# Kernel tuning notes

Measured on AMD Instinct MI355X. Metric: run time of the kernel, lower is better.

## Reference

```python
import jax, jax.numpy as jnp
import numpy as np

D = 256        # embedding_dim
K = 4096       # num_embeddings
DECAY = 0.99
EPS = 1e-05
COMMIT = 0.25


def setup_inputs() -> dict:
    key = jax.random.key(0)
    kx, ke = jax.random.split(key)
    x = jax.random.normal(kx, (32, 1024, D), dtype=jnp.float32)
    # variance_scaling(scale=1.0, mode='fan_in', distribution='uniform') on (D, K): fan_in = D
    limit = np.sqrt(3.0 / D).astype(np.float32)
    embeddings = jax.random.uniform(ke, (D, K), dtype=jnp.float32, minval=-limit, maxval=limit)
    return {
        'x': x,
        'embeddings': embeddings,
        'ema_counter': jnp.zeros((), jnp.float32),
        'ema_hidden_cluster': jnp.zeros((K,), jnp.float32),
        'ema_hidden_dw': jnp.zeros((D, K), jnp.float32),
    }


def reference(x, embeddings, ema_counter, ema_hidden_cluster, ema_hidden_dw):
    flat = x.reshape(-1, D)  # [N, D]
    # squared euclidean distance to each code: [N, K]
    distance = (jnp.sum(flat ** 2, axis=1, keepdims=True)
                - 2.0 * jnp.matmul(flat, embeddings)
                + jnp.sum(embeddings ** 2, axis=0, keepdims=True))
    encoding_indices = jnp.argmax(-distance, axis=1)           # [N]
    encodings = jax.nn.one_hot(encoding_indices, K, dtype=distance.dtype)  # [N, K]
    idx = encoding_indices.reshape(x.shape[:-1])               # [B, T]
    quantized = jnp.take(embeddings.T, idx, axis=0)            # [B, T, D]

    e_latent_loss = jnp.mean((quantized - x) ** 2)
    q_latent_loss = jnp.mean((quantized - x) ** 2)
    vq_loss = q_latent_loss + COMMIT * e_latent_loss

    # EMA codebook update (training=True path); debiased EMA per the module
    counter = ema_counter + 1.0
    bias = 1.0 - jnp.power(DECAY, counter)
    cluster_hidden = ema_hidden_cluster * DECAY + jnp.sum(encodings, axis=0) * (1.0 - DECAY)
    cluster_avg = cluster_hidden / bias                         # [K]
    dw = jnp.matmul(flat.T, encodings)                          # [D, K]
    dw_hidden = ema_hidden_dw * DECAY + dw * (1.0 - DECAY)
    dw_avg = dw_hidden / bias                                   # [D, K]
    n = jnp.sum(cluster_avg)
    cluster_norm = (cluster_avg + EPS) / (n + K * EPS) * n
    new_embeddings = dw_avg / cluster_norm[None, :]             # [D, K]

    avg_probs = jnp.mean(encodings, axis=0)
    perplexity = jnp.exp(-jnp.sum(avg_probs * jnp.log(avg_probs + 1e-10)))
    return quantized, vq_loss, perplexity, idx, new_embeddings
```

## Files before the change

### kernel.cpp

```cpp
#include <hip/hip_runtime.h>
#include <math.h>

#define N_TOK 32768
#define DIM   256
#define KCODE 4096

#define WS_E2      0
#define WS_COUNTS  4096
#define WS_LOSSP   8192
#define WS_SCAL    8448
#define WS_CNORM   8512
#define WS_IDX     12608
#define WS_EHS     307520
#define WS_DWT     1356096
#define WS_CARRYV  2404672
#define WS_CARRYI  2437440
#define WS_OFFS    2470208
#define WS_WOFF    2474304

#define OUT_Q      0
#define OUT_LOSS   8388608
#define OUT_PERP   8388609
#define OUT_IDX    8388610
#define OUT_EMB    8421378

#define EH_PLANE   1048576
#define XH_PLANE   8388608

typedef _Float16 f16x8 __attribute__((ext_vector_type(8)));
typedef _Float16 f16x4 __attribute__((ext_vector_type(4)));
typedef float    f32x4 __attribute__((ext_vector_type(4)));

__global__ void k_e2(const float* __restrict__ emb, float* __restrict__ e2)
{
    int k  = blockIdx.x * 256 + threadIdx.x;
    int d0 = blockIdx.y * 32;
    float s = 0.0f;
#pragma unroll 8
    for (int d = 0; d < 32; ++d) {
        float v = emb[(size_t)(d0 + d) * KCODE + k];
        s += v * v;
    }
    atomicAdd(&e2[k], s);
}

__global__ void k_split_x(const float* __restrict__ x, unsigned short* __restrict__ xh)
{
    int i = (blockIdx.x * 256 + threadIdx.x) * 8;
    float4 f0 = *(const float4*)(x + i);
    float4 f1 = *(const float4*)(x + i + 4);
    float fv[8] = {f0.x, f0.y, f0.z, f0.w, f1.x, f1.y, f1.z, f1.w};
    f16x8 h1, h2;
#pragma unroll
    for (int j = 0; j < 8; ++j) {
        _Float16 a = (_Float16)fv[j];
        h1[j] = a;
        h2[j] = (_Float16)(fv[j] - (float)a);
    }
    *(f16x8*)((_Float16*)xh + i)            = h1;
    *(f16x8*)((_Float16*)xh + XH_PLANE + i) = h2;
}

__global__ void k_split_e(const float* __restrict__ emb, unsigned short* __restrict__ ehs_)
{
    __shared__ float tile[32][33];
    _Float16* ehs = (_Float16*)ehs_;
    int t  = threadIdx.x;
    int tx = t & 31, iy = t >> 5;
    int k0 = blockIdx.x * 32, d0 = blockIdx.y * 32;
#pragma unroll
    for (int j = 0; j < 4; ++j)
        tile[iy + 8 * j][tx] = emb[(size_t)(d0 + iy + 8 * j) * KCODE + k0 + tx];
    __syncthreads();
    int code = k0 + tx;
    size_t base = (size_t)(((code >> 8) * 8) + (d0 >> 5)) * 8192 + (code & 255) * 32 + iy * 4;
    f16x4 h1, h2;
#pragma unroll
    for (int j = 0; j < 4; ++j) {
        float v = tile[iy * 4 + j][tx];
        _Float16 a = (_Float16)v;
        h1[j] = a;
        h2[j] = (_Float16)(v - (float)a);
    }
    *(f16x4*)(ehs + base)            = h1;
    *(f16x4*)(ehs + EH_PLANE + base) = h2;
}

__global__ __launch_bounds__(256, 2)
void k_argmin(const unsigned short* __restrict__ xh_, const unsigned short* __restrict__ ehs_,
              const float* __restrict__ e2, int* __restrict__ idx_out,
              float* __restrict__ carryV, int* __restrict__ carryI,
              float* __restrict__ out_idxf, float* __restrict__ counts,
              int ct0, int phase)
{
    __shared__ __align__(16) _Float16 Ah[2][64][256];

    const _Float16* xh  = (const _Float16*)xh_;
    const _Float16* ehs = (const _Float16*)ehs_;

    const int t    = threadIdx.x;
    const int lane = t & 63, w = t >> 6;
    const int lo   = lane & 15, q = lane >> 4;
    const int row0 = blockIdx.x * 64;

    {
        int m = t >> 3, kb = (t & 7) * 32;
#pragma unroll
        for (int p = 0; p < 2; ++p)
#pragma unroll
            for (int rr = 0; rr < 2; ++rr) {
                int mm = m + 32 * rr;
                const _Float16* src = xh + (size_t)p * XH_PLANE + (size_t)(row0 + mm) * DIM + kb;
#pragma unroll
                for (int g = 0; g < 4; ++g) {
                    f16x8 h = __builtin_nontemporal_load((const f16x8*)(src + g * 8));
                    int grp = ((kb >> 3) + g) ^ (mm & 7);
                    *(f16x8*)&Ah[p][mm][grp * 8] = h;
                }
            }
    }
    __syncthreads();

    float best[16];
    int   bidx[16];
#pragma unroll
    for (int s = 0; s < 16; ++s) { best[s] = 3.4e38f; bidx[s] = 0; }

    const _Float16* ehp1 = ehs + (size_t)(w * 64 + lo) * 32 + q * 8;
    const _Float16* ehp2 = ehp1 + EH_PLANE;

    f16x8 b1f[2][4], b2f[2][4];

    {
        const size_t so0 = (size_t)(ct0 * 8) * 8192;
#pragma unroll
        for (int nf = 0; nf < 4; ++nf) {
            b1f[0][nf] = *(const f16x8*)(ehp1 + so0 + nf * 512);
            b2f[0][nf] = *(const f16x8*)(ehp2 + so0 + nf * 512);
        }
    }

    for (int ct = ct0; ct < ct0 + 8; ++ct) {
        f32x4 acc[4][4];
#pragma unroll
        for (int mf = 0; mf < 4; ++mf)
#pragma unroll
            for (int nf = 0; nf < 4; ++nf) acc[mf][nf] = (f32x4)0.0f;

#pragma unroll
        for (int ks = 0; ks < 8; ++ks) {
            const int cur = ks & 1, nxt = cur ^ 1;
            const int so  = ct * 8 + ks;

            if (ks < 7 || ct < ct0 + 7) {
                const size_t po = (size_t)(so + 1) * 8192;
#pragma unroll
                for (int nf = 0; nf < 4; ++nf) {
                    b1f[nxt][nf] = *(const f16x8*)(ehp1 + po + nf * 512);
                    b2f[nxt][nf] = *(const f16x8*)(ehp2 + po + nf * 512);
                }
            }
            __builtin_amdgcn_sched_barrier(0);

            const int agrp = ((ks * 4 + q) ^ (lo & 7)) * 8;
            f16x8 a1[4], a2[4];
#pragma unroll
            for (int mf = 0; mf < 4; ++mf)
                a2[mf] = *(const f16x8*)&Ah[1][mf * 16 + lo][agrp];
#pragma unroll
            for (int mf = 0; mf < 4; ++mf)
                a1[mf] = *(const f16x8*)&Ah[0][mf * 16 + lo][agrp];

            __builtin_amdgcn_s_setprio(1);
#pragma unroll
            for (int nf = 0; nf < 4; ++nf) {
#pragma unroll
                for (int mf = 0; mf < 4; ++mf)
                    acc[mf][nf] = __builtin_amdgcn_mfma_f32_16x16x32_f16(a2[mf], b1f[cur][nf], acc[mf][nf], 0, 0, 0);
#pragma unroll
                for (int mf = 0; mf < 4; ++mf)
                    acc[mf][nf] = __builtin_amdgcn_mfma_f32_16x16x32_f16(a1[mf], b2f[cur][nf], acc[mf][nf], 0, 0, 0);
#pragma unroll
                for (int mf = 0; mf < 4; ++mf)
                    acc[mf][nf] = __builtin_amdgcn_mfma_f32_16x16x32_f16(a1[mf], b1f[cur][nf], acc[mf][nf], 0, 0, 0);
            }
            __builtin_amdgcn_s_setprio(0);
        }

#pragma unroll
        for (int nf = 0; nf < 4; ++nf) {
            int cl = w * 64 + nf * 16 + lo;
            float e2v = e2[ct * 256 + cl];
#pragma unroll
            for (int mf = 0; mf < 4; ++mf)
#pragma unroll
                for (int r = 0; r < 4; ++r) {
                    float dist = fmaf(-2.0f, acc[mf][nf][r], e2v);
                    int s = mf * 4 + r;
                    if (dist < best[s]) { best[s] = dist; bidx[s] = ct * 256 + cl; }
                }
        }
    }

    __syncthreads();
    float* rv = (float*)&Ah[0][0][0];
    int*   ri = (int*)(((char*)&Ah[0][0][0]) + 16384);
#pragma unroll
    for (int s = 0; s < 16; ++s) {
        int row = (s >> 2) * 16 + q * 4 + (s & 3);
        rv[row * 64 + w * 16 + lo] = best[s];
        ri[row * 64 + w * 16 + lo] = bidx[s];
    }
    __syncthreads();
    if (t < 64) {
        float bv; int bi;
        if (phase) { bv = carryV[row0 + t]; bi = carryI[row0 + t]; }
        else       { bv = 3.4e38f; bi = 0x40000000; }
        for (int jj = 0; jj < 64; ++jj) {
            int j = (jj + t) & 63;
            float v = rv[t * 64 + j];
            int  ii = ri[t * 64 + j];
            if (v < bv || (v == bv && ii < bi)) { bv = v; bi = ii; }
        }
        if (phase) {
            idx_out[row0 + t] = bi;
            out_idxf[row0 + t] = (float)bi;
            atomicAdd(&counts[bi], 1.0f);
        } else {
            carryV[row0 + t] = bv; carryI[row0 + t] = bi;
        }
    }
}

__global__ void k_scan(const float* __restrict__ counts, int* __restrict__ offs,
                       int* __restrict__ woff)
{
    __shared__ int ps[256];
    int t = threadIdx.x;
    int local[16];
    int s = 0;
#pragma unroll
    for (int j = 0; j < 16; ++j) {
        local[j] = s;
        s += (int)counts[t * 16 + j];
    }
    ps[t] = s;
    __syncthreads();
    for (int off = 1; off < 256; off <<= 1) {
        int v = (t >= off) ? ps[t - off] : 0;
        __syncthreads();
        ps[t] += v;
        __syncthreads();
    }
    int base = (t > 0) ? ps[t - 1] : 0;
#pragma unroll
    for (int j = 0; j < 16; ++j) {
        int o = base + local[j];
        offs[t * 16 + j] = o;
        woff[t * 16 + j] = o;
    }
}

__global__ void k_scatter(const int* __restrict__ idx, int* __restrict__ woff,
                          int* __restrict__ rowlist)
{
    int n = blockIdx.x * 256 + threadIdx.x;
    int k = idx[n];
    int pos = atomicAdd(&woff[k], 1);
    rowlist[pos] = n;
}

__global__ void k_dw(const float* __restrict__ x, const int* __restrict__ rowlist,
                     const int* __restrict__ offs, const float* __restrict__ counts,
                     float* __restrict__ dwT)
{
    __shared__ float red[4][256];
    int k = blockIdx.x;
    int t = threadIdx.x;
    int lane = t & 63, w = t >> 6;
    int start = offs[k];
    int cnt   = (int)counts[k];
    float4 acc = {0.0f, 0.0f, 0.0f, 0.0f};
    int j = w;
    for (; j + 4 < cnt; j += 8) {
        int n0 = rowlist[start + j];
        int n1 = rowlist[start + j + 4];
        float4 v0 = *(const float4*)&x[(size_t)n0 * DIM + lane * 4];
        float4 v1 = *(const float4*)&x[(size_t)n1 * DIM + lane * 4];
        acc.x += v0.x + v1.x; acc.y += v0.y + v1.y;
        acc.z += v0.z + v1.z; acc.w += v0.w + v1.w;
    }
    if (j < cnt) {
        int n0 = rowlist[start + j];
        float4 v0 = *(const float4*)&x[(size_t)n0 * DIM + lane * 4];
        acc.x += v0.x; acc.y += v0.y; acc.z += v0.z; acc.w += v0.w;
    }
    *(float4*)&red[w][lane * 4] = acc;
    __syncthreads();
    float s = red[0][t] + red[1][t] + red[2][t] + red[3][t];
    dwT[(size_t)k * DIM + t] = s;
}

__global__ void k_gather(const float* __restrict__ x, const unsigned short* __restrict__ ehs_,
                         const int* __restrict__ idx, float* __restrict__ out_q,
                         float* __restrict__ lossp)
{
    const _Float16* ehs = (const _Float16*)ehs_;
    int t = threadIdx.x;
    int lane = t & 63, w = t >> 6;
    int n = blockIdx.x * 4 + w;
    int k = idx[n];
    float4 xv = *(const float4*)&x[(size_t)n * DIM + lane * 4];
    size_t base = (size_t)(((k >> 8) * 8) + (lane >> 3)) * 8192 + (k & 255) * 32 + (lane & 7) * 4;
    f16x4 h1 = *(const f16x4*)(ehs + base);
    f16x4 h2 = *(const f16x4*)(ehs + EH_PLANE + base);
    float4 ev;
    ev.x = (float)h1[0] + (float)h2[0];
    ev.y = (float)h1[1] + (float)h2[1];
    ev.z = (float)h1[2] + (float)h2[2];
    ev.w = (float)h1[3] + (float)h2[3];
    *(float4*)&out_q[(size_t)n * DIM + lane * 4] = ev;
    float dx = ev.x - xv.x, dy = ev.y - xv.y, dz = ev.z - xv.z, dw = ev.w - xv.w;
    float s = dx * dx + dy * dy + dz * dz + dw * dw;
#pragma unroll
    for (int off = 32; off > 0; off >>= 1) s += __shfl_down(s, off, 64);
    if (lane == 0) atomicAdd(&lossp[blockIdx.x & 255], s);
}

__global__ void k_finalize(const float* __restrict__ counts, const float* __restrict__ lossp,
                           const float* __restrict__ ema_counter,
                           const float* __restrict__ ema_cluster,
                           float* __restrict__ cnorm, float* __restrict__ scal,
                           float* __restrict__ out)
{
    __shared__ float red[256];
    int t = threadIdx.x;
    float ls = lossp[t];
    float ent = 0.0f, casum = 0.0f;
    float ca[16];
#pragma unroll
    for (int j = 0; j < 16; ++j) {
        int k = j * 256 + t;
        float c = counts[k];
        float p = c * (1.0f / 32768.0f);
        ent += p * logf(p + 1e-10f);
        ca[j] = ema_cluster[k] * 0.99f + c * 0.01f;
        casum += ca[j];
    }
    red[t] = ls; __syncthreads();
    for (int o = 128; o > 0; o >>= 1) { if (t < o) red[t] += red[t + o]; __syncthreads(); }
    float loss_tot = red[0]; __syncthreads();
    red[t] = ent; __syncthreads();
    for (int o = 128; o > 0; o >>= 1) { if (t < o) red[t] += red[t + o]; __syncthreads(); }
    float ent_tot = red[0]; __syncthreads();
    red[t] = casum; __syncthreads();
    for (int o = 128; o > 0; o >>= 1) { if (t < o) red[t] += red[t + o]; __syncthreads(); }
    float casum_tot = red[0]; __syncthreads();

    float bias = 1.0f - powf(0.99f, ema_counter[0] + 1.0f);
    float n = casum_tot / bias;
    float inv = n / (n + 4096.0f * 1e-5f);
#pragma unroll
    for (int j = 0; j < 16; ++j) {
        int k = j * 256 + t;
        cnorm[k] = (ca[j] / bias + 1e-5f) * inv;
    }
    if (t == 0) {
        out[OUT_LOSS] = 1.25f * loss_tot * (1.0f / (32768.0f * 256.0f));
        out[OUT_PERP] = expf(-ent_tot);
        scal[0] = bias;
    }
}

__global__ void k_newemb(const float* __restrict__ dwT, const float* __restrict__ ema_dw,
                         const float* __restrict__ cnorm, const float* __restrict__ scal,
                         float* __restrict__ out_emb)
{
    __shared__ float tile[32][33];
    int t = threadIdx.x;
    int tx = t & 31, iy = t >> 5;
    int k0 = blockIdx.x * 32, d0 = blockIdx.y * 32;
#pragma unroll
    for (int j = 0; j < 4; ++j)
        tile[iy + 8 * j][tx] = dwT[(size_t)(k0 + iy + 8 * j) * DIM + d0 + tx];
    __syncthreads();
    float inv_bias = 1.0f / scal[0];
    float cn = cnorm[k0 + tx];
#pragma unroll
    for (int j = 0; j < 4; ++j) {
        int d = d0 + iy + 8 * j;
        float dwv = tile[tx][iy + 8 * j];
        float hid = ema_dw[(size_t)d * KCODE + k0 + tx] * 0.99f + dwv * 0.01f;
        out_emb[(size_t)d * KCODE + k0 + tx] = hid * inv_bias / cn;
    }
}

extern "C" void kernel_launch(void* const* d_in, const int* in_sizes, int n_in,
                              void* d_out, int out_size, void* d_ws, size_t ws_size,
                              hipStream_t stream)
{
    const float* x           = (const float*)d_in[0];
    const float* emb         = (const float*)d_in[1];
    const float* ema_counter = (const float*)d_in[2];
    const float* ema_cluster = (const float*)d_in[3];
    const float* ema_dw      = (const float*)d_in[4];
    float* out = (float*)d_out;
    float* ws  = (float*)d_ws;

    float* e2     = ws + WS_E2;
    float* counts = ws + WS_COUNTS;
    float* lossp  = ws + WS_LOSSP;
    float* scal   = ws + WS_SCAL;
    float* cnorm  = ws + WS_CNORM;
    int*   idxw   = (int*)(ws + WS_IDX);
    unsigned short* ehs = (unsigned short*)(ws + WS_EHS);
    float* dwT    = ws + WS_DWT;
    float* carryV = ws + WS_CARRYV;
    int*   carryI = (int*)(ws + WS_CARRYI);
    int*   rowlist= (int*)(ws + WS_CARRYV);
    int*   offs   = (int*)(ws + WS_OFFS);
    int*   woff   = (int*)(ws + WS_WOFF);
    unsigned short* xh = (unsigned short*)(out + OUT_Q);

    hipMemsetAsync(e2, 0, (size_t)WS_CNORM * sizeof(float), stream);

    k_e2<<<dim3(16, 8), 256, 0, stream>>>(emb, e2);
    k_split_e<<<dim3(128, 8), 256, 0, stream>>>(emb, ehs);
    k_split_x<<<4096, 256, 0, stream>>>(x, xh);
    k_argmin<<<512, 256, 0, stream>>>(xh, ehs, e2, idxw, carryV, carryI,
                                      out + OUT_IDX, counts, 0, 0);
    k_argmin<<<512, 256, 0, stream>>>(xh, ehs, e2, idxw, carryV, carryI,
                                      out + OUT_IDX, counts, 8, 1);
    k_gather<<<8192, 256, 0, stream>>>(x, ehs, idxw, out + OUT_Q, lossp);
    k_scan<<<1, 256, 0, stream>>>(counts, offs, woff);
    k_scatter<<<128, 256, 0, stream>>>(idxw, woff, rowlist);
    k_dw<<<4096, 256, 0, stream>>>(x, rowlist, offs, counts, dwT);
    k_finalize<<<1, 256, 0, stream>>>(counts, lossp, ema_counter, ema_cluster,
                                      cnorm, scal, out);
    k_newemb<<<dim3(128, 8), 256, 0, stream>>>(dwT, ema_dw, cnorm, scal, out + OUT_EMB);
}
```

Before: 363.6 us.

## Fuse x split into argmin, gather+loss into dw, e2 into split_e

Removes the separate x-to-fp16 split kernel by converting fp32 x to hi/lo fp16 planes directly while staging into shared memory in k_argmin. The quantized-output write and loss computation move into the per-code dw kernel, with the loss computed algebraically from cnt*|e|^2 - 2 e·sum(x) + sum|x|^2. The codeword norm computation is folded into k_split_e. Together these drop three launches and the xh round trip through memory. The cost is that x is now read at fp32 width twice, once per argmin pass, and the algebraic loss form can lose some float precision.

```diff
diff --git a/kernel.cpp b/kernel.cpp
--- a/kernel.cpp
+++ b/kernel.cpp
@@ -25,43 +25,13 @@
 #define OUT_EMB    8421378
 
 #define EH_PLANE   1048576
-#define XH_PLANE   8388608
 
 typedef _Float16 f16x8 __attribute__((ext_vector_type(8)));
 typedef _Float16 f16x4 __attribute__((ext_vector_type(4)));
 typedef float    f32x4 __attribute__((ext_vector_type(4)));
 
-__global__ void k_e2(const float* __restrict__ emb, float* __restrict__ e2)
-{
-    int k  = blockIdx.x * 256 + threadIdx.x;
-    int d0 = blockIdx.y * 32;
-    float s = 0.0f;
-#pragma unroll 8
-    for (int d = 0; d < 32; ++d) {
-        float v = emb[(size_t)(d0 + d) * KCODE + k];
-        s += v * v;
-    }
-    atomicAdd(&e2[k], s);
-}
-
-__global__ void k_split_x(const float* __restrict__ x, unsigned short* __restrict__ xh)
-{
-    int i = (blockIdx.x * 256 + threadIdx.x) * 8;
-    float4 f0 = *(const float4*)(x + i);
-    float4 f1 = *(const float4*)(x + i + 4);
-    float fv[8] = {f0.x, f0.y, f0.z, f0.w, f1.x, f1.y, f1.z, f1.w};
-    f16x8 h1, h2;
-#pragma unroll
-    for (int j = 0; j < 8; ++j) {
-        _Float16 a = (_Float16)fv[j];
-        h1[j] = a;
-        h2[j] = (_Float16)(fv[j] - (float)a);
-    }
-    *(f16x8*)((_Float16*)xh + i)            = h1;
-    *(f16x8*)((_Float16*)xh + XH_PLANE + i) = h2;
-}
-
-__global__ void k_split_e(const float* __restrict__ emb, unsigned short* __restrict__ ehs_)
+__global__ void k_split_e(const float* __restrict__ emb, unsigned short* __restrict__ ehs_,
+                          float* __restrict__ e2)
 {
     __shared__ float tile[32][33];
     _Float16* ehs = (_Float16*)ehs_;
@@ -75,19 +45,22 @@
     int code = k0 + tx;
     size_t base = (size_t)(((code >> 8) * 8) + (d0 >> 5)) * 8192 + (code & 255) * 32 + iy * 4;
     f16x4 h1, h2;
+    float ssq = 0.0f;
 #pragma unroll
     for (int j = 0; j < 4; ++j) {
         float v = tile[iy * 4 + j][tx];
+        ssq += v * v;
         _Float16 a = (_Float16)v;
         h1[j] = a;
         h2[j] = (_Float16)(v - (float)a);
     }
     *(f16x4*)(ehs + base)            = h1;
     *(f16x4*)(ehs + EH_PLANE + base) = h2;
+    atomicAdd(&e2[code], ssq);
 }
 
 __global__ __launch_bounds__(256, 2)
-void k_argmin(const unsigned short* __restrict__ xh_, const unsigned short* __restrict__ ehs_,
+void k_argmin(const float* __restrict__ x, const unsigned short* __restrict__ ehs_,
               const float* __restrict__ e2, int* __restrict__ idx_out,
               float* __restrict__ carryV, int* __restrict__ carryI,
               float* __restrict__ out_idxf, float* __restrict__ counts,
@@ -95,7 +68,6 @@
 {
     __shared__ __align__(16) _Float16 Ah[2][64][256];
 
-    const _Float16* xh  = (const _Float16*)xh_;
     const _Float16* ehs = (const _Float16*)ehs_;
 
     const int t    = threadIdx.x;
@@ -106,18 +78,26 @@
     {
         int m = t >> 3, kb = (t & 7) * 32;
 #pragma unroll
-        for (int p = 0; p < 2; ++p)
-#pragma unroll
-            for (int rr = 0; rr < 2; ++rr) {
-                int mm = m + 32 * rr;
-                const _Float16* src = xh + (size_t)p * XH_PLANE + (size_t)(row0 + mm) * DIM + kb;
-#pragma unroll
-                for (int g = 0; g < 4; ++g) {
-                    f16x8 h = __builtin_nontemporal_load((const f16x8*)(src + g * 8));
-                    int grp = ((kb >> 3) + g) ^ (mm & 7);
-                    *(f16x8*)&Ah[p][mm][grp * 8] = h;
+        for (int rr = 0; rr < 2; ++rr) {
+            int mm = m + 32 * rr;
+            const float* src = x + (size_t)(row0 + mm) * DIM + kb;
+#pragma unroll
+            for (int g = 0; g < 4; ++g) {
+                f32x4 f0 = __builtin_nontemporal_load((const f32x4*)(src + g * 8));
+                f32x4 f1 = __builtin_nontemporal_load((const f32x4*)(src + g * 8 + 4));
+                f16x8 h1, h2;
+#pragma unroll
+                for (int j = 0; j < 4; ++j) {
+                    _Float16 a = (_Float16)f0[j];
+                    h1[j] = a; h2[j] = (_Float16)(f0[j] - (float)a);
+                    _Float16 b = (_Float16)f1[j];
+                    h1[j + 4] = b; h2[j + 4] = (_Float16)(f1[j] - (float)b);
                 }
+                int grp = ((kb >> 3) + g) ^ (mm & 7);
+                *(f16x8*)&Ah[0][mm][grp * 8] = h1;
+                *(f16x8*)&Ah[1][mm][grp * 8] = h2;
             }
+        }
     }
     __syncthreads();
 
@@ -270,61 +250,54 @@
     rowlist[pos] = n;
 }
 
-__global__ void k_dw(const float* __restrict__ x, const int* __restrict__ rowlist,
-                     const int* __restrict__ offs, const float* __restrict__ counts,
-                     float* __restrict__ dwT)
-{
-    __shared__ float red[4][256];
-    int k = blockIdx.x;
-    int t = threadIdx.x;
+__global__ void k_dw(const float* __restrict__ x, const unsigned short* __restrict__ ehs_,
+                     const int* __restrict__ rowlist, const int* __restrict__ offs,
+                     const float* __restrict__ counts, float* __restrict__ dwT,
+                     float* __restrict__ out_q, float* __restrict__ lossp)
+{
+    __shared__ __align__(16) float es[256];
+    __shared__ __align__(16) float red[4][256];
+    const _Float16* ehs = (const _Float16*)ehs_;
+    int k = blockIdx.x, t = threadIdx.x;
     int lane = t & 63, w = t >> 6;
+    size_t base = (size_t)(((k >> 8) * 8) + (t >> 5)) * 8192 + (k & 255) * 32 + (t & 31);
+    float e = (float)ehs[base] + (float)ehs[EH_PLANE + base];
+    es[t] = e;
     int start = offs[k];
     int cnt   = (int)counts[k];
+    __syncthreads();
+    float4 ev = *(const float4*)&es[lane * 4];
     float4 acc = {0.0f, 0.0f, 0.0f, 0.0f};
-    int j = w;
-    for (; j + 4 < cnt; j += 8) {
-        int n0 = rowlist[start + j];
-        int n1 = rowlist[start + j + 4];
-        float4 v0 = *(const float4*)&x[(size_t)n0 * DIM + lane * 4];
-        float4 v1 = *(const float4*)&x[(size_t)n1 * DIM + lane * 4];
-        acc.x += v0.x + v1.x; acc.y += v0.y + v1.y;
-        acc.z += v0.z + v1.z; acc.w += v0.w + v1.w;
-    }
-    if (j < cnt) {
-        int n0 = rowlist[start + j];
-        float4 v0 = *(const float4*)&x[(size_t)n0 * DIM + lane * 4];
-        acc.x += v0.x; acc.y += v0.y; acc.z += v0.z; acc.w += v0.w;
+    float sq = 0.0f;
+    for (int j = w; j < cnt; j += 4) {
+        int n = rowlist[start + j];
+        float4 xv = *(const float4*)&x[(size_t)n * DIM + lane * 4];
+        acc.x += xv.x; acc.y += xv.y; acc.z += xv.z; acc.w += xv.w;
+        sq += xv.x * xv.x + xv.y * xv.y + xv.z * xv.z + xv.w * xv.w;
+        *(float4*)&out_q[(size_t)n * DIM + lane * 4] = ev;
     }
     *(float4*)&red[w][lane * 4] = acc;
     __syncthreads();
     float s = red[0][t] + red[1][t] + red[2][t] + red[3][t];
     dwT[(size_t)k * DIM + t] = s;
-}
-
-__global__ void k_gather(const float* __restrict__ x, const unsigned short* __restrict__ ehs_,
-                         const int* __restrict__ idx, float* __restrict__ out_q,
-                         float* __restrict__ lossp)
-{
-    const _Float16* ehs = (const _Float16*)ehs_;
-    int t = threadIdx.x;
-    int lane = t & 63, w = t >> 6;
-    int n = blockIdx.x * 4 + w;
-    int k = idx[n];
-    float4 xv = *(const float4*)&x[(size_t)n * DIM + lane * 4];
-    size_t base = (size_t)(((k >> 8) * 8) + (lane >> 3)) * 8192 + (k & 255) * 32 + (lane & 7) * 4;
-    f16x4 h1 = *(const f16x4*)(ehs + base);
-    f16x4 h2 = *(const f16x4*)(ehs + EH_PLANE + base);
-    float4 ev;
-    ev.x = (float)h1[0] + (float)h2[0];
-    ev.y = (float)h1[1] + (float)h2[1];
-    ev.z = (float)h1[2] + (float)h2[2];
-    ev.w = (float)h1[3] + (float)h2[3];
-    *(float4*)&out_q[(size_t)n * DIM + lane * 4] = ev;
-    float dx = ev.x - xv.x, dy = ev.y - xv.y, dz = ev.z - xv.z, dw = ev.w - xv.w;
-    float s = dx * dx + dy * dy + dz * dz + dw * dw;
-#pragma unroll
-    for (int off = 32; off > 0; off >>= 1) s += __shfl_down(s, off, 64);
-    if (lane == 0) atomicAdd(&lossp[blockIdx.x & 255], s);
+    float v1 = es[t] * s;
+    float v2 = e * e;
+    float v3 = sq;
+#pragma unroll
+    for (int off = 32; off > 0; off >>= 1) {
+        v1 += __shfl_down(v1, off, 64);
+        v2 += __shfl_down(v2, off, 64);
+        v3 += __shfl_down(v3, off, 64);
+    }
+    __syncthreads();
+    if (lane == 0) { red[0][w] = v1; red[1][w] = v2; red[2][w] = v3; }
+    __syncthreads();
+    if (t == 0 && cnt > 0) {
+        float dot = red[0][0] + red[0][1] + red[0][2] + red[0][3];
+        float e2t = red[1][0] + red[1][1] + red[1][2] + red[1][3];
+        float sqt = red[2][0] + red[2][1] + red[2][2] + red[2][3];
+        atomicAdd(&lossp[k & 255], (float)cnt * e2t - 2.0f * dot + sqt);
+    }
 }
 
 __global__ void k_finalize(const float* __restrict__ counts, const float* __restrict__ lossp,
@@ -420,21 +393,18 @@
     int*   rowlist= (int*)(ws + WS_CARRYV);
     int*   offs   = (int*)(ws + WS_OFFS);
     int*   woff   = (int*)(ws + WS_WOFF);
-    unsigned short* xh = (unsigned short*)(out + OUT_Q);
 
     hipMemsetAsync(e2, 0, (size_t)WS_CNORM * sizeof(float), stream);
 
-    k_e2<<<dim3(16, 8), 256, 0, stream>>>(emb, e2);
-    k_split_e<<<dim3(128, 8), 256, 0, stream>>>(emb, ehs);
-    k_split_x<<<4096, 256, 0, stream>>>(x, xh);
-    k_argmin<<<512, 256, 0, stream>>>(xh, ehs, e2, idxw, carryV, carryI,
+    k_split_e<<<dim3(128, 8), 256, 0, stream>>>(emb, ehs, e2);
+    k_argmin<<<512, 256, 0, stream>>>(x, ehs, e2, idxw, carryV, carryI,
                                       out + OUT_IDX, counts, 0, 0);
-    k_argmin<<<512, 256, 0, stream>>>(xh, ehs, e2, idxw, carryV, carryI,
+    k_argmin<<<512, 256, 0, stream>>>(x, ehs, e2, idxw, carryV, carryI,
                                       out + OUT_IDX, counts, 8, 1);
-    k_gather<<<8192, 256, 0, stream>>>(x, ehs, idxw, out + OUT_Q, lossp);
     k_scan<<<1, 256, 0, stream>>>(counts, offs, woff);
     k_scatter<<<128, 256, 0, stream>>>(idxw, woff, rowlist);
-    k_dw<<<4096, 256, 0, stream>>>(x, rowlist, offs, counts, dwT);
+    k_dw<<<4096, 256, 0, stream>>>(x, ehs, rowlist, offs, counts, dwT,
+                                   out + OUT_Q, lossp);
     k_finalize<<<1, 256, 0, stream>>>(counts, lossp, ema_counter, ema_cluster,
                                       cnorm, scal, out);
     k_newemb<<<dim3(128, 8), 256, 0, stream>>>(dwT, ema_dw, cnorm, scal, out + OUT_EMB);
```

Result: faster. 326.3 us (-10.3%).
